# Performance work log

Measured on AMD Instinct MI355X. Metric: run time of the kernel, lower is better.

The kernel has to match this reference:

```python
import jax, jax.numpy as jnp
import numpy as np
import math

# Shapes: b, coarse nodes, fine cells per coarse cell grouped as (seq_out, seq_in)
B, N_OUT, SO, SI, NV, NC = 4, 10240, 4, 4, 1, 32
N_PHI, N_DIST, N_SIGMA = 4, 4, 1
DIST_UNIT = 2.0  # (global_level_no - global_level_encode) * grid_layer_encode.nh_dist
MIN_SIGMA = 1e-10


def setup_inputs() -> dict:
    key = jax.random.key(0)
    k1, k2, k3 = jax.random.split(key, 3)
    n_in = N_OUT * SO * SI
    # x: (b, n_in, nh_in=1, nv, nc), nh_in_encode=False path (x.unsqueeze(2))
    x = jax.random.normal(k1, (B, n_in, 1, NV, NC), dtype=jnp.float32)
    # relative coordinates (cartesian, rotated frame): (1, n_out, seq_out, seq_in)
    coords_x = jax.random.uniform(k2, (1, N_OUT, SO, SI), dtype=jnp.float32,
                                  minval=-DIST_UNIT, maxval=DIST_UNIT)
    coords_y = jax.random.uniform(k3, (1, N_OUT, SO, SI), dtype=jnp.float32,
                                  minval=-DIST_UNIT, maxval=DIST_UNIT)
    # parameters exactly as in __init__
    phis = jnp.linspace(-jnp.pi, jnp.pi, N_PHI + 1)[:-1].astype(jnp.float32)
    d = jnp.arange(1, 2 * N_DIST, 2, dtype=jnp.float32) / (N_DIST * 2)
    dists_param = -jnp.log(1.0 / d - 1.0)  # inverse-sigmoid init
    s = 1.0 / (2 * N_DIST * math.sqrt(2 * math.log(2)))
    sigma_param = (-math.log(1.0 / s - 1.0)) * jnp.ones((N_SIGMA,), jnp.float32)
    return dict(x=x, coords_x=coords_x, coords_y=coords_y,
                phis=phis, dists_param=dists_param, sigma_param=sigma_param)


def reference(x, coords_x, coords_y, phis, dists_param, sigma_param):
    b = x.shape[0]
    nv, nc = x.shape[-2], x.shape[-1]
    n_out, so, si = coords_x.shape[1], coords_x.shape[2], coords_x.shape[3]

    # get_spatial_weights
    dists = DIST_UNIT * jax.nn.sigmoid(dists_param)              # (D,)
    mu_x = jnp.cos(phis)[:, None] * dists[None, :]               # (P, D)
    mu_y = jnp.sin(phis)[:, None] * dists[None, :]               # (P, D)
    sigma = jnp.maximum(DIST_UNIT * jax.nn.sigmoid(sigma_param), MIN_SIGMA)  # (S,)

    dx = coords_x[0][..., None, None] - mu_x                     # (O, so, si, P, D)
    dy = coords_y[0][..., None, None] - mu_y                     # (O, so, si, P, D)
    w = jnp.exp(-0.5 * (dx * dx + dy * dy)[..., None] / (sigma * sigma))  # (O, so, si, P, D, S)

    # mult_weights_t (n_out <= n_in branch): normalize over the (so, si) receptive field
    w = w / (w.sum(axis=(1, 2), keepdims=True) + 1e-20)

    # grouped view: n_in = n_out * so * si, nh_in = 1
    xr = x.reshape(b, n_out, so, si, nv, nc)
    # weighted reduce over the receptive field against mixture weights
    out = jnp.einsum('boijvc,oijpds->bovpdsc', xr, w)            # (b, O, nv, P, D, S, nc)
    return out
```

## Files before the change

### kernel.cpp

```cpp
#include <hip/hip_runtime.h>
#include <math.h>

namespace {

constexpr int NOUT = 10240;
constexpr int OW   = 4;
constexpr int NB   = 4;
constexpr int NIJ  = 16;
constexpr int NPD  = 16;
constexpr int NC   = 32;
constexpr int NIN  = NOUT * NIJ;
constexpr int WPAD = 20;

typedef float vfloat4 __attribute__((ext_vector_type(4)));

__device__ __forceinline__ void fma4(float4& a, float s, const float4& v) {
    a.x = fmaf(s, v.x, a.x);
    a.y = fmaf(s, v.y, a.y);
    a.z = fmaf(s, v.z, a.z);
    a.w = fmaf(s, v.w, a.w);
}

__device__ __forceinline__ void nt_store4(float4* p, const float4& v) {
    vfloat4 nv = { v.x, v.y, v.z, v.w };
    __builtin_nontemporal_store(nv, reinterpret_cast<vfloat4*>(p));
}

__global__ __launch_bounds__(256) void polnorm_kernel(
    const float* __restrict__ x,
    const float* __restrict__ cx,
    const float* __restrict__ cy,
    const float* __restrict__ phis,
    const float* __restrict__ dists_p,
    const float* __restrict__ sigma_p,
    float* __restrict__ out)
{
    __shared__ __align__(16) float s_w[OW][NPD][WPAD];
    __shared__ __align__(16) float s_x[OW][NIJ * NC];

    const int t   = threadIdx.x;
    const int wid = t >> 6;
    const int l   = t & 63;
    const int c4  = l & 7;
    const int pda = l >> 3;

    const int o = blockIdx.x * OW + wid;

    const float4* xg = reinterpret_cast<const float4*>(x) + (size_t)o * (NIJ * NC / 4);
    float4*       og = reinterpret_cast<float4*>(out)     + (size_t)o * (NPD * NC / 4);
    const size_t xstride = (size_t)NIN * NC / 4;
    const size_t ostride = (size_t)NOUT * NPD * NC / 4;

    float4 f0 = xg[l];
    float4 f1 = xg[64 + l];
    float4 g0 = xg[xstride + l];
    float4 g1 = xg[xstride + 64 + l];

    float inv0, inv1;
    {
        const int pdf = l >> 2;
        const int ijq = (l & 3) * 4;
        const int p = pdf >> 2, dd = pdf & 3;

        const float dist = 2.0f / (1.0f + expf(-dists_p[dd]));
        const float phi  = phis[p];
        const float mux  = cosf(phi) * dist;
        const float muy  = sinf(phi) * dist;
        float sg = 2.0f / (1.0f + expf(-sigma_p[0]));
        sg = fmaxf(sg, 1e-10f);
        const float coef = -0.5f / (sg * sg);

        const float4 cxi = *reinterpret_cast<const float4*>(&cx[o * NIJ + ijq]);
        const float4 cyi = *reinterpret_cast<const float4*>(&cy[o * NIJ + ijq]);

        float4 w;
        { float dx = cxi.x - mux, dy = cyi.x - muy; w.x = expf(coef * (dx*dx + dy*dy)); }
        { float dx = cxi.y - mux, dy = cyi.y - muy; w.y = expf(coef * (dx*dx + dy*dy)); }
        { float dx = cxi.z - mux, dy = cyi.z - muy; w.z = expf(coef * (dx*dx + dy*dy)); }
        { float dx = cxi.w - mux, dy = cyi.w - muy; w.w = expf(coef * (dx*dx + dy*dy)); }

        float s = w.x + w.y + w.z + w.w;
        s += __shfl_xor(s, 1);
        s += __shfl_xor(s, 2);
        const float inv = 1.0f / (s + 1e-20f);

        *reinterpret_cast<float4*>(&s_w[wid][pdf][ijq]) = w;

        inv0 = __shfl(inv, pda * 4);
        inv1 = __shfl(inv, pda * 4 + 32);
    }

    float4* xs = reinterpret_cast<float4*>(s_x[wid]);

    #pragma unroll
    for (int bi = 0; bi < NB; ++bi) {
        xs[l] = f0;
        xs[64 + l] = f1;

        f0 = g0; f1 = g1;
        if (bi + 2 < NB) {
            g0 = xg[(size_t)(bi + 2) * xstride + l];
            g1 = xg[(size_t)(bi + 2) * xstride + 64 + l];
        }

        float4 acc0 = make_float4(0.f, 0.f, 0.f, 0.f);
        float4 acc1 = make_float4(0.f, 0.f, 0.f, 0.f);

        #pragma unroll
        for (int kk = 0; kk < 4; ++kk) {
            const float4 wa = *reinterpret_cast<const float4*>(&s_w[wid][pda][kk * 4]);
            const float4 wb = *reinterpret_cast<const float4*>(&s_w[wid][pda + 8][kk * 4]);
            const float4 xv0 = xs[(kk * 4 + 0) * 8 + c4];
            const float4 xv1 = xs[(kk * 4 + 1) * 8 + c4];
            const float4 xv2 = xs[(kk * 4 + 2) * 8 + c4];
            const float4 xv3 = xs[(kk * 4 + 3) * 8 + c4];
            fma4(acc0, wa.x, xv0); fma4(acc1, wb.x, xv0);
            fma4(acc0, wa.y, xv1); fma4(acc1, wb.y, xv1);
            fma4(acc0, wa.z, xv2); fma4(acc1, wb.z, xv2);
            fma4(acc0, wa.w, xv3); fma4(acc1, wb.w, xv3);
        }

        acc0.x *= inv0; acc0.y *= inv0; acc0.z *= inv0; acc0.w *= inv0;
        acc1.x *= inv1; acc1.y *= inv1; acc1.z *= inv1; acc1.w *= inv1;

        nt_store4(&og[(size_t)bi * ostride + l], acc0);
        nt_store4(&og[(size_t)bi * ostride + 64 + l], acc1);
    }
}

}

extern "C" void kernel_launch(void* const* d_in, const int* in_sizes, int n_in,
                              void* d_out, int out_size, void* d_ws, size_t ws_size,
                              hipStream_t stream) {
    const float* x  = (const float*)d_in[0];
    const float* cx = (const float*)d_in[1];
    const float* cy = (const float*)d_in[2];
    const float* ph = (const float*)d_in[3];
    const float* dp = (const float*)d_in[4];
    const float* sp = (const float*)d_in[5];
    float* out = (float*)d_out;

    dim3 grid(NOUT / OW);
    dim3 block(256);
    hipLaunchKernelGGL(polnorm_kernel, grid, block, 0, stream,
                       x, cx, cy, ph, dp, sp, out);
}
```

Measured before the change: 33.37 us.

## Issue all batch loads of x upfront and hoist weight reads into registers

```diff
diff --git a/kernel.cpp b/kernel.cpp
--- a/kernel.cpp
+++ b/kernel.cpp
@@ -51,10 +51,12 @@
     const size_t xstride = (size_t)NIN * NC / 4;
     const size_t ostride = (size_t)NOUT * NPD * NC / 4;
 
-    float4 f0 = xg[l];
-    float4 f1 = xg[64 + l];
-    float4 g0 = xg[xstride + l];
-    float4 g1 = xg[xstride + 64 + l];
+    float4 x0[NB], x1[NB];
+    #pragma unroll
+    for (int bi = 0; bi < NB; ++bi) {
+        x0[bi] = xg[(size_t)bi * xstride + l];
+        x1[bi] = xg[(size_t)bi * xstride + 64 + l];
+    }
 
     float inv0, inv1;
     {
@@ -90,34 +92,33 @@
         inv1 = __shfl(inv, pda * 4 + 32);
     }
 
+    float4 wa[4], wb[4];
+    #pragma unroll
+    for (int kk = 0; kk < 4; ++kk) {
+        wa[kk] = *reinterpret_cast<const float4*>(&s_w[wid][pda][kk * 4]);
+        wb[kk] = *reinterpret_cast<const float4*>(&s_w[wid][pda + 8][kk * 4]);
+    }
+
     float4* xs = reinterpret_cast<float4*>(s_x[wid]);
 
     #pragma unroll
     for (int bi = 0; bi < NB; ++bi) {
-        xs[l] = f0;
-        xs[64 + l] = f1;
-
-        f0 = g0; f1 = g1;
-        if (bi + 2 < NB) {
-            g0 = xg[(size_t)(bi + 2) * xstride + l];
-            g1 = xg[(size_t)(bi + 2) * xstride + 64 + l];
-        }
+        xs[l] = x0[bi];
+        xs[64 + l] = x1[bi];
 
         float4 acc0 = make_float4(0.f, 0.f, 0.f, 0.f);
         float4 acc1 = make_float4(0.f, 0.f, 0.f, 0.f);
 
         #pragma unroll
         for (int kk = 0; kk < 4; ++kk) {
-            const float4 wa = *reinterpret_cast<const float4*>(&s_w[wid][pda][kk * 4]);
-            const float4 wb = *reinterpret_cast<const float4*>(&s_w[wid][pda + 8][kk * 4]);
             const float4 xv0 = xs[(kk * 4 + 0) * 8 + c4];
             const float4 xv1 = xs[(kk * 4 + 1) * 8 + c4];
             const float4 xv2 = xs[(kk * 4 + 2) * 8 + c4];
             const float4 xv3 = xs[(kk * 4 + 3) * 8 + c4];
-            fma4(acc0, wa.x, xv0); fma4(acc1, wb.x, xv0);
-            fma4(acc0, wa.y, xv1); fma4(acc1, wb.y, xv1);
-            fma4(acc0, wa.z, xv2); fma4(acc1, wb.z, xv2);
-            fma4(acc0, wa.w, xv3); fma4(acc1, wb.w, xv3);
+            fma4(acc0, wa[kk].x, xv0); fma4(acc1, wb[kk].x, xv0);
+            fma4(acc0, wa[kk].y, xv1); fma4(acc1, wb[kk].y, xv1);
+            fma4(acc0, wa[kk].z, xv2); fma4(acc1, wb[kk].z, xv2);
+            fma4(acc0, wa[kk].w, xv3); fma4(acc1, wb[kk].w, xv3);
         }
 
         acc0.x *= inv0; acc0.y *= inv0; acc0.z *= inv0; acc0.w *= inv0;
```

Measured after the change: 30.89 us (median of 2 runs). -7.4%, faster.
